# Kernel optimization log

Measured on AMD Instinct MI355X. Metric: run time of the kernel, lower is better.

## Reference

```python
import jax, jax.numpy as jnp
import numpy as np

D = 64      # node_input_dim == node_hidden_dim
EIN = 16    # edge_input_dim
EH = 64     # edge_hidden_dim
NL, NR = 5000, 15000
EL, ER = 50000, 150000
STEPS = 6
EPS = 1e-5
SLOPE = 0.01


def _ln(x, g, b):
    mu = jnp.mean(x, axis=-1, keepdims=True)
    v = jnp.mean((x - mu) ** 2, axis=-1, keepdims=True)
    return (x - mu) / jnp.sqrt(v + EPS) * g + b


def _lrelu(x):
    return jnp.where(x > 0, x, SLOPE * x)


def setup_inputs() -> dict:
    key = jax.random.key(0)
    ks = jax.random.split(key, 32)

    def n(k, shape, fan_in):
        return jax.random.normal(k, shape, jnp.float32) * (fan_in ** -0.5)

    return {
        'lig_n_feat': jax.random.normal(ks[0], (NL, D), jnp.float32),
        'lig_e_feat': jax.random.normal(ks[1], (EL, EIN), jnp.float32),
        'lig_src': jax.random.randint(ks[2], (EL,), 0, NL),
        'lig_dst': jax.random.randint(ks[3], (EL,), 0, NL),
        'rec_n_feat': jax.random.normal(ks[4], (NR, D), jnp.float32),
        'rec_e_feat': jax.random.normal(ks[5], (ER, EIN), jnp.float32),
        'rec_src': jax.random.randint(ks[6], (ER,), 0, NR),
        'rec_dst': jax.random.randint(ks[7], (ER,), 0, NR),
        'mask': jax.random.uniform(ks[8], (NL, NR), jnp.float32),
        # linear0
        'W0': n(ks[9], (D, D), D), 'b0': jnp.zeros((D,), jnp.float32),
        # edge network: Linear(EIN,EH) -> ReLU -> Linear(EH, D*D)
        'We1': n(ks[10], (EH, EIN), EIN), 'be1': jnp.zeros((EH,), jnp.float32),
        'We2': n(ks[11], (D * D, EH), EH), 'be2': jnp.zeros((D * D,), jnp.float32),
        # NNConv residual fc (no bias) and conv bias
        'resW': n(ks[12], (D, D), D), 'conv_b': jnp.zeros((D,), jnp.float32),
        # message layer Linear(2D, D)
        'msgW': n(ks[13], (D, 2 * D), 2 * D), 'msgb': jnp.zeros((D,), jnp.float32),
        # attention projections (no bias)
        'Qlig': n(ks[14], (D, D), D), 'Klig': n(ks[15], (D, D), D), 'Vlig': n(ks[16], (D, D), D),
        'Qrec': n(ks[17], (D, D), D), 'Krec': n(ks[18], (D, D), D), 'Vrec': n(ks[19], (D, D), D),
        # final LayerNorms
        'g_lig': jnp.ones((D,), jnp.float32), 'b_lig': jnp.zeros((D,), jnp.float32),
        'g_rec': jnp.ones((D,), jnp.float32), 'b_rec': jnp.zeros((D,), jnp.float32),
    }


def _gather_branch(x, efeat, src, dst, n_nodes, W0, b0, We1, be1, We2, be2, resW, conv_b, msgW, msgb):
    # per-edge weight matrices from edge MLP: [E, D, D] (in x out)
    We = jax.nn.relu(efeat @ We1.T + be1) @ We2.T + be2
    We = We.reshape(-1, D, D)
    h = jax.nn.relu(x @ W0.T + b0)
    for _ in range(STEPS):
        msg = jnp.einsum('ei,eio->eo', h[src], We)          # gather + per-edge transform
        agg = jax.ops.segment_sum(msg, dst, num_segments=n_nodes)  # scatter-sum
        m = jax.nn.relu(agg + h @ resW.T + conv_b)           # NNConv residual + bias, relu
        h = jnp.concatenate([m, h], axis=1) @ msgW.T + msgb  # message_layer
    return h + x


def reference(lig_n_feat, lig_e_feat, lig_src, lig_dst, rec_n_feat, rec_e_feat, rec_src, rec_dst,
              mask, W0, b0, We1, be1, We2, be2, resW, conv_b, msgW, msgb,
              Qlig, Klig, Vlig, Qrec, Krec, Vrec, g_lig, b_lig, g_rec, b_rec):
    lig_Fv = _gather_branch(lig_n_feat, lig_e_feat, lig_src, lig_dst, NL,
                            W0, b0, We1, be1, We2, be2, resW, conv_b, msgW, msgb)
    rec_Fv = _gather_branch(rec_n_feat, rec_e_feat, rec_src, rec_dst, NR,
                            W0, b0, We1, be1, We2, be2, resW, conv_b, msgW, msgb)
    hl = _ln(lig_Fv, g_lig, b_lig)
    hr = _ln(rec_Fv, g_rec, b_rec)
    # lig attends to rec
    ql, kr, vr = _lrelu(hl @ Qlig.T), _lrelu(hr @ Krec.T), hr @ Vrec.T
    a = mask * (ql @ kr.T) - 1000.0 * (1.0 - mask)
    att_lig = jax.nn.softmax(a, axis=1) @ vr
    # rec attends to lig
    qr, kl, vl = _lrelu(hr @ Qrec.T), _lrelu(hl @ Klig.T), hl @ Vlig.T
    mt = mask.T
    a2 = mt * (qr @ kl.T) - 1000.0 * (1.0 - mt)
    att_rec = jax.nn.softmax(a2, axis=1) @ vl
    return (_ln(att_lig, g_lig, b_lig), _ln(att_rec, g_rec, b_rec))
```

## Files before the change

### kernel.cpp

```cpp
#include <hip/hip_runtime.h>
#include <hip/hip_bf16.h>

typedef unsigned short ushort_t;
typedef __attribute__((ext_vector_type(8))) short short8_t;
typedef __attribute__((ext_vector_type(4))) float f32x4;
typedef __attribute__((ext_vector_type(4))) unsigned uint4_t;
typedef __attribute__((ext_vector_type(2))) unsigned uint2_t;

#define NLIG 5000
#define NREC 15000
#define NTOT 20000
#define ELIG 50000
#define EREC 150000
#define ETOT 200000
#define VSTRIDE 20160
#define NB0 313
#define NB1 938
#define SEGLEN 5000
#define NBA (NB0*3 + NB1)
#define PSLOT 1056

__device__ __forceinline__ float us2f(ushort_t u){
  union { float f; unsigned int i; } x; x.i = ((unsigned int)u) << 16; return x.f;
}
__device__ __forceinline__ ushort_t f2us(float f){
  __hip_bfloat16 b = __float2bfloat16(f);
  return *reinterpret_cast<ushort_t*>(&b);
}
__device__ __forceinline__ unsigned pkbf(float a, float b){
  return (unsigned)f2us(a) | ((unsigned)f2us(b) << 16);
}
__device__ __forceinline__ float wsum64(float v){
#pragma unroll
  for (int s = 32; s >= 1; s >>= 1) v += __shfl_xor(v, s, 64);
  return v;
}
__device__ __forceinline__ f32x4 mfma32(short8_t a, short8_t b, f32x4 c){
  return __builtin_amdgcn_mfma_f32_16x16x32_bf16(a, b, c, 0, 0, 0);
}
__device__ __forceinline__ int geti(const int* __restrict__ p, int i, int i64){
  return i64 ? p[2*i] : p[i];
}

__global__ void kdetect2(const unsigned* __restrict__ xw, const unsigned* __restrict__ iw,
                         int* __restrict__ flagp){
  const int lane = threadIdx.x;
  unsigned w = xw[lane];
  int e0 = (int)((w >> 7) & 0xFF);
  int hit = (e0 >= 100 && e0 <= 134) ? 1 : 0;
  int zodd = ((lane & 1) && iw[lane] == 0u) ? 1 : 0;
#pragma unroll
  for (int s = 32; s >= 1; s >>= 1){
    hit  += __shfl_xor(hit,  s, 64);
    zodd += __shfl_xor(zodd, s, 64);
  }
  if (lane == 0){
    flagp[0] = (hit  >= 40) ? 1 : 0;
    flagp[1] = (zodd >= 24) ? 1 : 0;
  }
}

__global__ void ksent(float* __restrict__ out, int n, float c){
  int i = blockIdx.x*256 + threadIdx.x;
  if (i < n) out[i] = c;
}

__global__ void kcvt_x(const void* __restrict__ lx, const void* __restrict__ rx,
                       const int* __restrict__ flagp, float* __restrict__ xall){
  const int flag = flagp[0];
  const int idx = blockIdx.x*256 + threadIdx.x;
  const void* src; int local;
  if (idx < NLIG*64){ src = lx; local = idx; } else { src = rx; local = idx - NLIG*64; }
  float v;
  if (flag) v = us2f(((const ushort_t*)src)[local]);
  else      v = ((const float*)src)[local];
  xall[idx] = v;
}

struct Srcs { const void* p[20]; };
__global__ void kcvt_w(Srcs S, const int* __restrict__ flagp, float* __restrict__ wcvt){
  const int bounds[21] = {0,4096,4160,5184,5248,267392,271488,275584,275648,283840,
                          283904,288000,292096,296192,300288,304384,308480,308544,308608,308672,308736};
  const int flag = flagp[0];
  const int idx = blockIdx.x*256 + threadIdx.x;
  if (idx >= 308736) return;
  int seg = 0;
#pragma unroll
  for (int s = 1; s < 20; ++s) if (idx >= bounds[s]) seg = s;
  const void* src = S.p[0];
#pragma unroll
  for (int s = 1; s < 20; ++s) if (seg == s) src = S.p[s];
  const int local = idx - bounds[seg];
  float v;
  if (flag) v = us2f(((const ushort_t*)src)[local]);
  else      v = ((const float*)src)[local];
  wcvt[idx] = v;
}

#define W_W0    0
#define W_B0    4096
#define W_WE1   4160
#define W_BE1   5184
#define W_WE2   5248
#define W_BE2   267392
#define W_RESW  271488
#define W_CONVB 275584
#define W_MSGW  275648
#define W_MSGB  283840
#define W_QLIG  283904
#define W_KLIG  288000
#define W_VLIG  292096
#define W_QREC  296192
#define W_KREC  300288
#define W_VREC  304384
#define W_GLIG  308480
#define W_BLIG  308544
#define W_GREC  308608
#define W_BREC  308672

__global__ void kWpk(const float* __restrict__ We2f, ushort_t* __restrict__ Wpk){
  int oidx = blockIdx.x*256 + threadIdx.x;
  int j = oidx & 7, lane = (oidx >> 3) & 63, p = (oidx >> 9) & 1;
  int t = (oidx >> 10) & 3, kb = oidx >> 12;
  int o = t*16 + (lane & 15);
  int gik = kb*32 + (lane >> 4)*8 + j;
  int i = gik >> 6, k = gik & 63;
  float v = We2f[(size_t)(i*64 + o)*64 + k];
  ushort_t hi = f2us(v);
  Wpk[oidx] = p ? f2us(v - us2f(hi)) : hi;
}

__global__ void kh0(const float* __restrict__ xall, const float* __restrict__ W0f,
                    const float* __restrict__ b0f, float* __restrict__ h){
  __shared__ float xr[4][64];
  const int lane = threadIdx.x & 63, wv = threadIdx.x >> 6;
  const int n = blockIdx.x*4 + wv;
  xr[wv][lane] = xall[(size_t)n*64 + lane];
  __syncthreads();
  float acc = b0f[lane];
  const float* wr = W0f + lane*64;
#pragma unroll
  for (int i = 0; i < 64; ++i) acc += xr[wv][i] * wr[i];
  h[(size_t)n*64 + lane] = acc > 0.f ? acc : 0.f;
}

__global__ void khist(const int* __restrict__ ldst, const int* __restrict__ rdst,
                      const int* __restrict__ flagp, int* __restrict__ counts){
  const int i64 = flagp[1];
  const int e = blockIdx.x*256 + threadIdx.x;
  if (e >= ETOT) return;
  int dstg = (e < ELIG) ? geti(ldst, e, i64) : geti(rdst, e - ELIG, i64) + NLIG;
  atomicAdd(&counts[dstg], 1);
}

__global__ __launch_bounds__(1024) void kscan(const int* __restrict__ counts, int* __restrict__ offs){
  __shared__ int part[1024];
  const int tid = threadIdx.x;
  const int PER = 20;
  int loc[PER]; int s = 0;
#pragma unroll
  for (int j = 0; j < PER; ++j){ int idx = tid*PER + j; int v = (idx < NTOT) ? counts[idx] : 0; loc[j] = s; s += v; }
  part[tid] = s;
  __syncthreads();
  for (int d = 1; d < 1024; d <<= 1){
    int add = (tid >= d) ? part[tid - d] : 0;
    __syncthreads();
    part[tid] += add;
    __syncthreads();
  }
  int pre = (tid > 0) ? part[tid - 1] : 0;
#pragma unroll
  for (int j = 0; j < PER; ++j){ int idx = tid*PER + j; if (idx < NTOT) offs[idx] = pre + loc[j]; }
  if (tid == 1023) offs[NTOT] = part[1023];
}

__global__ void kfill(const int* __restrict__ lsrc, const int* __restrict__ ldst,
                      const int* __restrict__ rsrc, const int* __restrict__ rdst,
                      const void* __restrict__ lef, const void* __restrict__ ref_,
                      const int* __restrict__ offs, int* __restrict__ cursor,
                      const int* __restrict__ flagp,
                      int* __restrict__ e_srcn, float* __restrict__ ef_srt){
  const int flag = flagp[0];
  const int i64  = flagp[1];
  const int e = blockIdx.x*256 + threadIdx.x;
  if (e >= ETOT) return;
  int srcg, dstg, le; const void* efb;
  if (e < ELIG){ srcg = geti(lsrc, e, i64); dstg = geti(ldst, e, i64); efb = lef; le = e; }
  else {
    int e2 = e - ELIG;
    srcg = geti(rsrc, e2, i64) + NLIG; dstg = geti(rdst, e2, i64) + NLIG; efb = ref_; le = e2;
  }
  int pos = offs[dstg] + atomicAdd(&cursor[dstg], 1);
  e_srcn[pos] = srcg;
  float* efd = ef_srt + (size_t)pos*16;
  if (flag){
    const ushort_t* efp = (const ushort_t*)efb + (size_t)le*16;
#pragma unroll
    for (int c = 0; c < 16; ++c) efd[c] = us2f(efp[c]);
  } else {
    const float* efp = (const float*)efb + (size_t)le*16;
#pragma unroll
    for (int c = 0; c < 16; ++c) efd[c] = efp[c];
  }
}

__global__ void kz(const float* __restrict__ ef_srt, const float* __restrict__ We1f,
                   const float* __restrict__ be1f, float* __restrict__ z_srt){
  const int lane = threadIdx.x & 63, wv = threadIdx.x >> 6;
  const int e = blockIdx.x*4 + wv;
  const float* efp = ef_srt + (size_t)e*16;
  float acc = be1f[lane];
  const float* wr = We1f + lane*16;
#pragma unroll
  for (int c = 0; c < 16; ++c) acc += efp[c] * wr[c];
  z_srt[(size_t)e*64 + lane] = acc > 0.f ? acc : 0.f;
}

#define SROW 2080
#define SLO  (16*SROW)
__global__ __launch_bounds__(1024)
void kstep(const float* __restrict__ hin, float* __restrict__ hout,
           const int* __restrict__ offs, const int* __restrict__ e_srcn,
           const float* __restrict__ z_srt,
           const ushort_t* __restrict__ Wpk,
           const float* __restrict__ resWf, const float* __restrict__ convbf,
           const float* __restrict__ msgWf, const float* __restrict__ msgbf,
           const float* __restrict__ be2f){
  __shared__ alignas(16) char sbuf[2*SLO];
  __shared__ float h_lds[1024];
  __shared__ float Hs_lds[1024];
  __shared__ float m_lds[1024];
  __shared__ float cbf[64], mbf[64];

  const int tid = threadIdx.x, lane = tid & 63, wv = tid >> 6;
  const int n0 = blockIdx.x * 16;

  h_lds[tid] = hin[(size_t)n0*64 + tid];
  if (tid < 64){ cbf[tid] = convbf[tid]; mbf[tid] = msgbf[tid]; }

  float sacc[64];
#pragma unroll
  for (int i = 0; i < 64; ++i) sacc[i] = 0.f;
  float hs = 0.f;
  {
    const int v = n0 + wv;
    const int jb = offs[v], je = offs[v+1];
    for (int j = jb; j < je; ++j){
      const int sn = e_srcn[j];
      const float zl = z_srt[(size_t)j*64 + lane];
      hs += hin[(size_t)sn*64 + lane];
      const float4* hp = (const float4*)(hin + (size_t)sn*64);
#pragma unroll
      for (int i4 = 0; i4 < 16; ++i4){
        float4 hv = hp[i4];
        sacc[i4*4+0] += hv.x * zl;
        sacc[i4*4+1] += hv.y * zl;
        sacc[i4*4+2] += hv.z * zl;
        sacc[i4*4+3] += hv.w * zl;
      }
    }
    Hs_lds[wv*64 + lane] = hs;
  }

  const int r15 = lane & 15, g4 = lane >> 4;
  const int tW = wv & 3, kq = wv >> 2;
  f32x4 acc; acc[0]=0.f; acc[1]=0.f; acc[2]=0.f; acc[3]=0.f;
#pragma unroll
  for (int c = 0; c < 4; ++c){
#pragma unroll
    for (int ii = 0; ii < 16; ++ii){
      float v = sacc[c*16 + ii];
      ushort_t hi16 = f2us(v);
      unsigned off = (unsigned)(wv*SROW + (ii*64 + lane)*2);
      *(ushort_t*)(sbuf + off) = hi16;
      *(ushort_t*)(sbuf + SLO + off) = f2us(v - us2f(hi16));
    }
    __syncthreads();
    for (int kk = 0; kk < 8; ++kk){
      const int lk = kq*256 + kk*32;
      const int kb = c*32 + kq*8 + kk;
      const unsigned aoff = (unsigned)(r15*SROW + (lk + g4*8)*2);
      const short8_t ah = *(const short8_t*)(sbuf + aoff);
      const short8_t al = *(const short8_t*)(sbuf + SLO + aoff);
      const ushort_t* bp = Wpk + (size_t)(kb*4 + tW)*1024 + lane*8;
      const short8_t bh = *(const short8_t*)(bp);
      const short8_t bl = *(const short8_t*)(bp + 512);
      acc = mfma32(ah, bh, acc);
      acc = mfma32(ah, bl, acc);
      acc = mfma32(al, bh, acc);
    }
    __syncthreads();
  }

  float* redf  = (float*)sbuf;
  float* be2s  = (float*)(sbuf + 16384);
  float* resWt = (float*)(sbuf + 32768);
#pragma unroll
  for (int q = 0; q < 4; ++q)
    redf[kq*1024 + (g4*4 + q)*64 + tW*16 + r15] = acc[q];
  for (int idx = tid; idx < 4096; idx += 1024){
    be2s[idx] = be2f[idx];
    resWt[(idx & 63)*65 + (idx >> 6)] = resWf[idx];
  }
  __syncthreads();
  {
    float aggv = cbf[lane];
#pragma unroll
    for (int k4 = 0; k4 < 4; ++k4) aggv += redf[k4*1024 + wv*64 + lane];
    float t1 = 0.f, t2 = 0.f;
#pragma unroll 8
    for (int i = 0; i < 64; ++i){
      t1 += Hs_lds[wv*64 + i] * be2s[i*64 + lane];
      t2 += h_lds[wv*64 + i]  * resWt[i*65 + lane];
    }
    float mv = aggv + t1 + t2;
    m_lds[wv*64 + lane] = mv > 0.f ? mv : 0.f;
  }
  __syncthreads();
  float* msgWt = (float*)sbuf;
  for (int idx = tid; idx < 8192; idx += 1024)
    msgWt[(idx & 127)*65 + (idx >> 7)] = msgWf[idx];
  __syncthreads();
  {
    float hn = mbf[lane];
#pragma unroll 8
    for (int i = 0; i < 64; ++i){
      hn += m_lds[wv*64 + i] * msgWt[i*65 + lane];
      hn += h_lds[wv*64 + i] * msgWt[(64 + i)*65 + lane];
    }
    hout[(size_t)(n0 + wv)*64 + lane] = hn;
  }
}

__global__ void kfvproj(const float* __restrict__ h, const float* __restrict__ xall,
    const float* __restrict__ wcvt,
    ushort_t* __restrict__ qbh, ushort_t* __restrict__ qbl,
    ushort_t* __restrict__ kbh, ushort_t* __restrict__ kbl,
    ushort_t* __restrict__ vbT){
  __shared__ float hr[4][64];
  const int lane = threadIdx.x & 63, wv = threadIdx.x >> 6;
  const int n = blockIdx.x*4 + wv;
  const bool isLig = n < NLIG;
  const float fv = h[(size_t)n*64 + lane] + xall[(size_t)n*64 + lane];
  const float mu = wsum64(fv) * (1.f/64.f);
  const float dd = fv - mu;
  const float var = wsum64(dd*dd) * (1.f/64.f);
  const float gg = wcvt[(isLig ? W_GLIG : W_GREC) + lane];
  const float bb = wcvt[(isLig ? W_BLIG : W_BREC) + lane];
  const float hl = dd * rsqrtf(var + 1e-5f) * gg + bb;
  hr[wv][lane] = hl;
  __syncthreads();
  const float* Qw = wcvt + (isLig ? W_QLIG : W_QREC) + lane*64;
  const float* Kw = wcvt + (isLig ? W_KLIG : W_KREC) + lane*64;
  const float* Vw = wcvt + (isLig ? W_VLIG : W_VREC) + lane*64;
  float qa = 0.f, ka = 0.f, va = 0.f;
#pragma unroll
  for (int i = 0; i < 64; ++i){
    const float hv = hr[wv][i];
    qa += hv * Qw[i];
    ka += hv * Kw[i];
    va += hv * Vw[i];
  }
  qa = qa > 0.f ? qa : 0.01f*qa;
  ka = ka > 0.f ? ka : 0.01f*ka;
  const size_t o = (size_t)n*64 + lane;
  ushort_t qh = f2us(qa); qbh[o] = qh; qbl[o] = f2us(qa - us2f(qh));
  ushort_t kh = f2us(ka); kbh[o] = kh; kbl[o] = f2us(ka - us2f(kh));
  vbT[(size_t)lane*VSTRIDE + n] = f2us(va);
}

__global__ __launch_bounds__(512)
void kattn4(const ushort_t* __restrict__ qbh, const ushort_t* __restrict__ qbl,
            const ushort_t* __restrict__ kbh, const ushort_t* __restrict__ kbl,
            const ushort_t* __restrict__ vbT, const void* __restrict__ maskp,
            const int* __restrict__ flagp, float* __restrict__ pbuf){
  __shared__ float slab[8][2][512];

  const int flag = flagp[0];
  const int tid = threadIdx.x, lane = tid & 63, wv = tid >> 6;
  const int gw = blockIdx.x*8 + wv;
  if (gw >= NBA) return;
  const int dirn = (gw < NB0*3) ? 0 : 1;
  const int bid  = dirn ? (gw - NB0*3) : (gw/3);
  const int seg  = dirn ? 0 : (gw - (gw/3)*3);
  const int R   = dirn ? NREC : NLIG;
  const int C   = dirn ? NLIG : NREC;
  const int RNB = dirn ? NLIG : 0;
  const int CNB = dirn ? 0 : NLIG;
  const int cs  = dirn ? 0 : seg*SEGLEN;
  const int ce  = dirn ? C : (cs + SEGLEN);

  const int r15 = lane & 15, g4 = lane >> 4;
  const int rbase = bid*16;
  int rn = rbase + r15; if (rn > R-1) rn = R-1;

  const ushort_t* qph = qbh + (size_t)(RNB + rn)*64;
  const ushort_t* qpl = qbl + (size_t)(RNB + rn)*64;
  const short8_t qh0a = *(const short8_t*)(qph + g4*8);
  const short8_t qh0b = *(const short8_t*)(qph + 32 + g4*8);
  const short8_t ql0a = *(const short8_t*)(qpl + g4*8);
  const short8_t ql0b = *(const short8_t*)(qpl + 32 + g4*8);

  const int srcA = (((g4 & 1) * 2)     << 4) + r15;
  const int srcB = (((g4 & 1) * 2 + 1) << 4) + r15;
  const bool hiBank = (g4 >> 1) != 0;

  auto d0_load = [&](int cb, float4 &va, float4 &vb){
    int cA = cb + g4*4;      if (cA > C-4) cA = C-4;
    int cB = cb + 16 + g4*4; if (cB > C-4) cB = C-4;
    if (flag){
      const ushort_t* mrow = (const ushort_t*)maskp + (size_t)rn*NREC;
      const uint2_t wa = *(const uint2_t*)(mrow + cA);
      const uint2_t wb = *(const uint2_t*)(mrow + cB);
      va.x = us2f((ushort_t)(wa[0] & 0xFFFF)); va.y = us2f((ushort_t)(wa[0] >> 16));
      va.z = us2f((ushort_t)(wa[1] & 0xFFFF)); va.w = us2f((ushort_t)(wa[1] >> 16));
      vb.x = us2f((ushort_t)(wb[0] & 0xFFFF)); vb.y = us2f((ushort_t)(wb[0] >> 16));
      vb.z = us2f((ushort_t)(wb[1] & 0xFFFF)); vb.w = us2f((ushort_t)(wb[1] >> 16));
    } else {
      const float* mrow = (const float*)maskp + (size_t)rn*NREC;
      va = *(const float4*)(mrow + cA);
      vb = *(const float4*)(mrow + cB);
    }
  };
  const int s_c = lane >> 1, s_h = lane & 1;
  auto d1_load = [&](int cb, float4 &va, float4 &vb){
    int c = cb + s_c; if (c > C-1) c = C-1;
    int r0 = rbase + s_h*8; if (r0 > R-8) r0 = R-8;
    const size_t base = (size_t)c*NREC + r0;
    if (flag){
      const ushort_t* mp = (const ushort_t*)maskp + base;
      const short8_t v8 = *(const short8_t*)mp;
      va.x = us2f((ushort_t)v8[0]); va.y = us2f((ushort_t)v8[1]);
      va.z = us2f((ushort_t)v8[2]); va.w = us2f((ushort_t)v8[3]);
      vb.x = us2f((ushort_t)v8[4]); vb.y = us2f((ushort_t)v8[5]);
      vb.z = us2f((ushort_t)v8[6]); vb.w = us2f((ushort_t)v8[7]);
    } else {
      const float* mp = (const float*)maskp + base;
      va = *(const float4*)mp;
      vb = *(const float4*)(mp + 4);
    }
  };
  auto d1_write = [&](int b, const float4 &va, const float4 &vb){
    float* s = &slab[wv][b][s_c*16 + s_h*8];
    *(float4*)s = va; *(float4*)(s + 4) = vb;
  };

  float mrun = -1e30f, lrun = 0.f;
  f32x4 oacc[4];
#pragma unroll
  for (int t = 0; t < 4; ++t){ oacc[t][0]=0.f; oacc[t][1]=0.f; oacc[t][2]=0.f; oacc[t][3]=0.f; }

  float4 pA, pB;
  if (dirn == 0) d0_load(cs, pA, pB);
  else { d1_load(cs, pA, pB); d1_write(0, pA, pB); d1_load(cs + 32, pA, pB); }

  int buf = 0;
  for (int cb = cs; cb < ce; cb += 32){
    float mv0[4], mv1[4];
    if (dirn == 0){
      mv0[0]=pA.x; mv0[1]=pA.y; mv0[2]=pA.z; mv0[3]=pA.w;
      mv1[0]=pB.x; mv1[1]=pB.y; mv1[2]=pB.z; mv1[3]=pB.w;
      if (cb + 32 < ce) d0_load(cb + 32, pA, pB);
    } else {
      const float* s = &slab[wv][buf][0];
#pragma unroll
      for (int j = 0; j < 4; ++j){
        mv0[j] = s[(g4*4 + j)*16 + r15];
        mv1[j] = s[(16 + g4*4 + j)*16 + r15];
      }
      if (cb + 32 < ce){
        d1_write(buf ^ 1, pA, pB);
        if (cb + 64 < ce) d1_load(cb + 64, pA, pB);
      }
      buf ^= 1;
    }

    int cn0 = cb + r15;      if (cn0 > C-1) cn0 = C-1;
    int cn1 = cb + 16 + r15; if (cn1 > C-1) cn1 = C-1;
    const ushort_t* kp0h = kbh + (size_t)(CNB + cn0)*64;
    const ushort_t* kp0l = kbl + (size_t)(CNB + cn0)*64;
    const ushort_t* kp1h = kbh + (size_t)(CNB + cn1)*64;
    const ushort_t* kp1l = kbl + (size_t)(CNB + cn1)*64;
    f32x4 st0; st0[0]=0.f; st0[1]=0.f; st0[2]=0.f; st0[3]=0.f;
    f32x4 st1 = st0;
    {
      short8_t ka_ = *(const short8_t*)(kp0h + g4*8);
      short8_t kb_ = *(const short8_t*)(kp0h + 32 + g4*8);
      st0 = mfma32(ka_, qh0a, st0); st0 = mfma32(kb_, qh0b, st0);
      st0 = mfma32(ka_, ql0a, st0); st0 = mfma32(kb_, ql0b, st0);
      short8_t kc_ = *(const short8_t*)(kp0l + g4*8);
      short8_t kd_ = *(const short8_t*)(kp0l + 32 + g4*8);
      st0 = mfma32(kc_, qh0a, st0); st0 = mfma32(kd_, qh0b, st0);
    }
    {
      short8_t ka_ = *(const short8_t*)(kp1h + g4*8);
      short8_t kb_ = *(const short8_t*)(kp1h + 32 + g4*8);
      st1 = mfma32(ka_, qh0a, st1); st1 = mfma32(kb_, qh0b, st1);
      st1 = mfma32(ka_, ql0a, st1); st1 = mfma32(kb_, ql0b, st1);
      short8_t kc_ = *(const short8_t*)(kp1l + g4*8);
      short8_t kd_ = *(const short8_t*)(kp1l + 32 + g4*8);
      st1 = mfma32(kc_, qh0a, st1); st1 = mfma32(kd_, qh0b, st1);
    }
    float sv0[4], sv1[4]; float tmax = -1e30f;
#pragma unroll
    for (int j = 0; j < 4; ++j){
      const int c0 = cb + g4*4 + j, c1 = cb + 16 + g4*4 + j;
      sv0[j] = (c0 < ce) ? mv0[j] * (st0[j] + 1000.f) : -1e30f;
      sv1[j] = (c1 < ce) ? mv1[j] * (st1[j] + 1000.f) : -1e30f;
      tmax = fmaxf(tmax, fmaxf(sv0[j], sv1[j]));
    }
    tmax = fmaxf(tmax, __shfl_xor(tmax, 16, 64));
    tmax = fmaxf(tmax, __shfl_xor(tmax, 32, 64));
    const float mnew = fmaxf(mrun, tmax);
    const float corr = __expf(mrun - mnew);
    float ps0[4], ps1[4], psum = 0.f;
#pragma unroll
    for (int j = 0; j < 4; ++j){
      ps0[j] = __expf(sv0[j] - mnew); psum += ps0[j];
      ps1[j] = __expf(sv1[j] - mnew); psum += ps1[j];
    }
    psum += __shfl_xor(psum, 16, 64);
    psum += __shfl_xor(psum, 32, 64);
    lrun = lrun * corr + psum;
    mrun = mnew;
    const unsigned pk0 = pkbf(ps0[0], ps0[1]);
    const unsigned pk1 = pkbf(ps0[2], ps0[3]);
    const unsigned pk2 = pkbf(ps1[0], ps1[1]);
    const unsigned pk3 = pkbf(ps1[2], ps1[3]);
    const unsigned a0 = (unsigned)__shfl((int)pk0, srcA, 64);
    const unsigned a2 = (unsigned)__shfl((int)pk2, srcA, 64);
    const unsigned a1 = (unsigned)__shfl((int)pk1, srcA, 64);
    const unsigned a3 = (unsigned)__shfl((int)pk3, srcA, 64);
    const unsigned b0 = (unsigned)__shfl((int)pk0, srcB, 64);
    const unsigned b2 = (unsigned)__shfl((int)pk2, srcB, 64);
    const unsigned b1 = (unsigned)__shfl((int)pk1, srcB, 64);
    const unsigned b3 = (unsigned)__shfl((int)pk3, srcB, 64);
    uint4_t pw;
    pw[0] = hiBank ? a2 : a0;
    pw[1] = hiBank ? a3 : a1;
    pw[2] = hiBank ? b2 : b0;
    pw[3] = hiBank ? b3 : b1;
    const short8_t pf8 = *reinterpret_cast<const short8_t*>(&pw);
    const ushort_t* vtb = vbT + (size_t)(CNB + cb + g4*8);
#pragma unroll
    for (int t = 0; t < 4; ++t){
#pragma unroll
      for (int q = 0; q < 4; ++q) oacc[t][q] *= corr;
      const short8_t af = *(const short8_t*)(vtb + (size_t)(t*16 + r15)*VSTRIDE);
      oacc[t] = mfma32(af, pf8, oacc[t]);
    }
  }

  float* ps = pbuf + (size_t)gw * PSLOT;
  if (g4 == 0){ ps[r15] = mrun; ps[16 + r15] = lrun; }
#pragma unroll
  for (int t = 0; t < 4; ++t)
#pragma unroll
    for (int q = 0; q < 4; ++q)
      ps[32 + r15*64 + t*16 + g4*4 + q] = oacc[t][q];
}

__global__ __launch_bounds__(64)
void kcomb(const float* __restrict__ pbuf, const float* __restrict__ wcvt,
           float* __restrict__ out){
  const int rb = blockIdx.x;
  const int lane = threadIdx.x;
  const int dirn = (rb < NB0) ? 0 : 1;
  const int bid  = dirn ? (rb - NB0) : rb;
  const int R    = dirn ? NREC : NLIG;
  const int nseg = dirn ? 1 : 3;
  const int slot0= dirn ? (NB0*3 + bid) : (bid*3);
  const float* gwf = wcvt + (dirn ? W_GREC : W_GLIG);
  const float* bwf = wcvt + (dirn ? W_BREC : W_BLIG);
  float* outp = out + (size_t)(dirn ? NLIG : 0)*64;
  const int rbase = bid * 16;

  for (int rr = 0; rr < 16; ++rr){
    const int rg = rbase + rr;
    if (rg >= R) break;
    float mstar = -1e30f;
    for (int s = 0; s < nseg; ++s)
      mstar = fmaxf(mstar, pbuf[(size_t)(slot0 + s)*PSLOT + rr]);
    float lstar = 0.f, ov = 0.f;
    for (int s = 0; s < nseg; ++s){
      const float* psl = pbuf + (size_t)(slot0 + s)*PSLOT;
      const float e = __expf(psl[rr] - mstar);
      lstar += psl[16 + rr] * e;
      ov    += psl[32 + rr*64 + lane] * e;
    }
    const float att = ov / lstar;
    const float mu = wsum64(att) * (1.f/64.f);
    const float dd = att - mu;
    const float var = wsum64(dd*dd) * (1.f/64.f);
    const float y = dd * rsqrtf(var + 1e-5f) * gwf[lane] + bwf[lane];
    outp[(size_t)rg*64 + lane] = y;
  }
}

extern "C" void kernel_launch(void* const* d_in, const int* in_sizes, int n_in,
                              void* d_out, int out_size, void* d_ws, size_t ws_size,
                              hipStream_t stream){
  const int expsz[29] = {320000,800000,50000,50000,960000,2400000,150000,150000,75000000,
                         4096,64,1024,64,262144,4096,4096,64,8192,64,
                         4096,4096,4096,4096,4096,4096,64,64,64,64};
  bool ok = (n_in == 29);
  if (ok) for (int i = 0; i < 29; ++i) if (in_sizes[i] != expsz[i]) ok = false;
  if (!ok){
    ksent<<<(out_size + 255)/256, 256, 0, stream>>>((float*)d_out, out_size, 10.0f);
    return;
  }

  const void* lig_n = d_in[0];
  const void* lig_e = d_in[1];
  const int* lig_src = (const int*)d_in[2];
  const int* lig_dst = (const int*)d_in[3];
  const void* rec_n = d_in[4];
  const void* rec_e = d_in[5];
  const int* rec_src = (const int*)d_in[6];
  const int* rec_dst = (const int*)d_in[7];
  const void* mask = d_in[8];

  char* p = (char*)d_ws;
  auto carve = [&](size_t bytes)->char*{ char* r = p; p += (bytes + 255) & ~(size_t)255; return r; };
  float*    xall  = (float*)   carve((size_t)NTOT*64*4);
  float*    wcvt  = (float*)   carve((size_t)308736*4);
  float*    h_a   = (float*)   carve((size_t)NTOT*64*4);
  float*    h_b   = (float*)   carve((size_t)NTOT*64*4);
  ushort_t* Wpk   = (ushort_t*)carve((size_t)524288*2);
  ushort_t* qbh   = (ushort_t*)carve((size_t)NTOT*64*2);
  ushort_t* qbl   = (ushort_t*)carve((size_t)NTOT*64*2);
  ushort_t* kbh   = (ushort_t*)carve((size_t)NTOT*64*2);
  ushort_t* kbl   = (ushort_t*)carve((size_t)NTOT*64*2);
  ushort_t* vbT   = (ushort_t*)carve((size_t)64*VSTRIDE*2);
  int*      flag  = (int*)     carve(256);
  int*      counts= (int*)     carve((size_t)2*NTOT*4);
  int*      cursor= counts + NTOT;
  int*      offs  = (int*)     carve((size_t)(NTOT+1)*4);
  int*      e_srcn= (int*)     carve((size_t)ETOT*4);
  float*    ef_srt= (float*)   carve((size_t)ETOT*16*4);
  float*    z_srt = (float*)   carve((size_t)ETOT*64*4);
  float*    pbuf  = ef_srt;

  if ((size_t)(p - (char*)d_ws) > ws_size){
    ksent<<<(out_size + 255)/256, 256, 0, stream>>>((float*)d_out, out_size, 20.0f);
    return;
  }

  Srcs S;
  for (int i = 0; i < 20; ++i) S.p[i] = d_in[9 + i];

  hipMemsetAsync(counts, 0, (size_t)2*NTOT*4, stream);
  hipMemsetAsync(vbT, 0, (size_t)64*VSTRIDE*2, stream);
  kdetect2<<<1, 64, 0, stream>>>((const unsigned*)lig_n, (const unsigned*)lig_src, flag);
  kcvt_x<<<NTOT*64/256, 256, 0, stream>>>(lig_n, rec_n, flag, xall);
  kcvt_w<<<(308736 + 255)/256, 256, 0, stream>>>(S, flag, wcvt);
  kWpk<<<2048, 256, 0, stream>>>(wcvt + W_WE2, Wpk);
  kh0<<<NTOT/4, 256, 0, stream>>>(xall, wcvt + W_W0, wcvt + W_B0, h_a);
  khist<<<(ETOT + 255)/256, 256, 0, stream>>>(lig_dst, rec_dst, flag, counts);
  kscan<<<1, 1024, 0, stream>>>(counts, offs);
  kfill<<<(ETOT + 255)/256, 256, 0, stream>>>(lig_src, lig_dst, rec_src, rec_dst,
                                              lig_e, rec_e, offs, cursor, flag, e_srcn, ef_srt);
  kz<<<ETOT/4, 256, 0, stream>>>(ef_srt, wcvt + W_WE1, wcvt + W_BE1, z_srt);
  float* hi = h_a; float* ho = h_b;
  for (int s = 0; s < 6; ++s){
    kstep<<<NTOT/16, 1024, 0, stream>>>(hi, ho, offs, e_srcn, z_srt, Wpk,
                                        wcvt + W_RESW, wcvt + W_CONVB,
                                        wcvt + W_MSGW, wcvt + W_MSGB, wcvt + W_BE2);
    float* t = hi; hi = ho; ho = t;
  }
  kfvproj<<<NTOT/4, 256, 0, stream>>>(hi, xall, wcvt, qbh, qbl, kbh, kbl, vbT);
  kattn4<<<(NBA + 7)/8, 512, 0, stream>>>(qbh, qbl, kbh, kbl, vbT, mask, flag, pbuf);
  kcomb<<<NB0 + NB1, 64, 0, stream>>>(pbuf, wcvt, (float*)d_out);
}
```

Measured before the change: 2.153 ms.

## Tile V into 32-column blocks, XCD-aware attention scheduling, four-way segment split

Stores the transposed V in 32-column tiles of 2048 elements so each MFMA A-operand load reads a contiguous 4 KB block instead of rows strided by 20160 elements. The attention launch is reorganised into a fixed 320-block grid that uses blockIdx low bits (assumed to map to XCDs) to pick direction and column segment, and the lig->rec direction is split into four segments instead of three. Mask prefetch for the next tile is moved after the MFMA work. Aims for better cache locality and load balance, at the cost of more partial-softmax slots for kcomb to merge.

```diff
diff --git a/kernel.cpp b/kernel.cpp
--- a/kernel.cpp
+++ b/kernel.cpp
@@ -13,12 +13,14 @@
 #define ELIG 50000
 #define EREC 150000
 #define ETOT 200000
-#define VSTRIDE 20160
 #define NB0 313
 #define NB1 938
-#define SEGLEN 5000
-#define NBA (NB0*3 + NB1)
+#define SEG0LEN 3744
+#define NBA2 (NB0*4 + NB1)
 #define PSLOT 1056
+#define VT_LIG 0
+#define VT_REC 157
+#define VT_NT  626
 
 __device__ __forceinline__ float us2f(ushort_t u){
   union { float f; unsigned int i; } x; x.i = ((unsigned int)u) << 16; return x.f;
@@ -336,7 +338,7 @@
     const float* __restrict__ wcvt,
     ushort_t* __restrict__ qbh, ushort_t* __restrict__ qbl,
     ushort_t* __restrict__ kbh, ushort_t* __restrict__ kbl,
-    ushort_t* __restrict__ vbT){
+    ushort_t* __restrict__ vbT3){
   __shared__ float hr[4][64];
   const int lane = threadIdx.x & 63, wv = threadIdx.x >> 6;
   const int n = blockIdx.x*4 + wv;
@@ -366,32 +368,42 @@
   const size_t o = (size_t)n*64 + lane;
   ushort_t qh = f2us(qa); qbh[o] = qh; qbl[o] = f2us(qa - us2f(qh));
   ushort_t kh = f2us(ka); kbh[o] = kh; kbl[o] = f2us(ka - us2f(kh));
-  vbT[(size_t)lane*VSTRIDE + n] = f2us(va);
+  const int c   = isLig ? n : (n - NLIG);
+  const int cbb = (isLig ? VT_LIG : VT_REC) + (c >> 5);
+  vbT3[(size_t)cbb*2048 + lane*32 + (c & 31)] = f2us(va);
 }
 
 __global__ __launch_bounds__(512)
-void kattn4(const ushort_t* __restrict__ qbh, const ushort_t* __restrict__ qbl,
+void kattn5(const ushort_t* __restrict__ qbh, const ushort_t* __restrict__ qbl,
             const ushort_t* __restrict__ kbh, const ushort_t* __restrict__ kbl,
-            const ushort_t* __restrict__ vbT, const void* __restrict__ maskp,
+            const ushort_t* __restrict__ vbT3, const void* __restrict__ maskp,
             const int* __restrict__ flagp, float* __restrict__ pbuf){
   __shared__ float slab[8][2][512];
 
   const int flag = flagp[0];
   const int tid = threadIdx.x, lane = tid & 63, wv = tid >> 6;
-  const int gw = blockIdx.x*8 + wv;
-  if (gw >= NBA) return;
-  const int dirn = (gw < NB0*3) ? 0 : 1;
-  const int bid  = dirn ? (gw - NB0*3) : (gw/3);
-  const int seg  = dirn ? 0 : (gw - (gw/3)*3);
-  const int R   = dirn ? NREC : NLIG;
-  const int C   = dirn ? NLIG : NREC;
-  const int RNB = dirn ? NLIG : 0;
-  const int CNB = dirn ? 0 : NLIG;
-  const int cs  = dirn ? 0 : seg*SEGLEN;
-  const int ce  = dirn ? C : (cs + SEGLEN);
+  const int b = blockIdx.x, xcd = b & 7, kslot = b >> 3;
+
+  int dirn, rb, slot, cs, ce, C, CNB, RNB, R, cbbase;
+  if (xcd < 4){
+    dirn = 0;
+    rb = kslot*8 + wv;
+    if (rb >= NB0) return;
+    slot = rb*4 + xcd;
+    cs = xcd*SEG0LEN;
+    ce = (xcd == 3) ? NREC : cs + SEG0LEN;
+    C = NREC; CNB = NLIG; RNB = 0; R = NLIG; cbbase = VT_REC;
+  } else {
+    dirn = 1;
+    int j = (kslot*8 + wv)*4 + (xcd - 4);
+    if (j >= NB1) return;
+    rb = j; slot = NB0*4 + j;
+    cs = 0; ce = NLIG;
+    C = NLIG; CNB = 0; RNB = NLIG; R = NREC; cbbase = VT_LIG;
+  }
 
   const int r15 = lane & 15, g4 = lane >> 4;
-  const int rbase = bid*16;
+  const int rbase = rb*16;
   int rn = rbase + r15; if (rn > R-1) rn = R-1;
 
   const ushort_t* qph = qbh + (size_t)(RNB + rn)*64;
@@ -440,8 +452,8 @@
       vb = *(const float4*)(mp + 4);
     }
   };
-  auto d1_write = [&](int b, const float4 &va, const float4 &vb){
-    float* s = &slab[wv][b][s_c*16 + s_h*8];
+  auto d1_write = [&](int bq, const float4 &va, const float4 &vb){
+    float* s = &slab[wv][bq][s_c*16 + s_h*8];
     *(float4*)s = va; *(float4*)(s + 4) = vb;
   };
 
@@ -460,7 +472,6 @@
     if (dirn == 0){
       mv0[0]=pA.x; mv0[1]=pA.y; mv0[2]=pA.z; mv0[3]=pA.w;
       mv1[0]=pB.x; mv1[1]=pB.y; mv1[2]=pB.z; mv1[3]=pB.w;
-      if (cb + 32 < ce) d0_load(cb + 32, pA, pB);
     } else {
       const float* s = &slab[wv][buf][0];
 #pragma unroll
@@ -468,11 +479,6 @@
         mv0[j] = s[(g4*4 + j)*16 + r15];
         mv1[j] = s[(16 + g4*4 + j)*16 + r15];
       }
-      if (cb + 32 < ce){
-        d1_write(buf ^ 1, pA, pB);
-        if (cb + 64 < ce) d1_load(cb + 64, pA, pB);
-      }
-      buf ^= 1;
     }
 
     int cn0 = cb + r15;      if (cn0 > C-1) cn0 = C-1;
@@ -541,17 +547,26 @@
     pw[2] = hiBank ? b2 : b0;
     pw[3] = hiBank ? b3 : b1;
     const short8_t pf8 = *reinterpret_cast<const short8_t*>(&pw);
-    const ushort_t* vtb = vbT + (size_t)(CNB + cb + g4*8);
+    const ushort_t* vtb = vbT3 + (size_t)(cbbase + (cb >> 5))*2048 + g4*8;
 #pragma unroll
     for (int t = 0; t < 4; ++t){
 #pragma unroll
       for (int q = 0; q < 4; ++q) oacc[t][q] *= corr;
-      const short8_t af = *(const short8_t*)(vtb + (size_t)(t*16 + r15)*VSTRIDE);
+      const short8_t af = *(const short8_t*)(vtb + (t*16 + r15)*32);
       oacc[t] = mfma32(af, pf8, oacc[t]);
     }
-  }
-
-  float* ps = pbuf + (size_t)gw * PSLOT;
+    if (dirn == 0){
+      if (cb + 32 < ce) d0_load(cb + 32, pA, pB);
+    } else {
+      if (cb + 32 < ce){
+        d1_write(buf ^ 1, pA, pB);
+        if (cb + 64 < ce) d1_load(cb + 64, pA, pB);
+      }
+      buf ^= 1;
+    }
+  }
+
+  float* ps = pbuf + (size_t)slot * PSLOT;
   if (g4 == 0){ ps[r15] = mrun; ps[16 + r15] = lrun; }
 #pragma unroll
   for (int t = 0; t < 4; ++t)
@@ -568,8 +583,8 @@
   const int dirn = (rb < NB0) ? 0 : 1;
   const int bid  = dirn ? (rb - NB0) : rb;
   const int R    = dirn ? NREC : NLIG;
-  const int nseg = dirn ? 1 : 3;
-  const int slot0= dirn ? (NB0*3 + bid) : (bid*3);
+  const int nseg = dirn ? 1 : 4;
+  const int slot0= dirn ? (NB0*4 + bid) : (bid*4);
   const float* gwf = wcvt + (dirn ? W_GREC : W_GLIG);
   const float* bwf = wcvt + (dirn ? W_BREC : W_BLIG);
   float* outp = out + (size_t)(dirn ? NLIG : 0)*64;
@@ -631,7 +646,7 @@
   ushort_t* qbl   = (ushort_t*)carve((size_t)NTOT*64*2);
   ushort_t* kbh   = (ushort_t*)carve((size_t)NTOT*64*2);
   ushort_t* kbl   = (ushort_t*)carve((size_t)NTOT*64*2);
-  ushort_t* vbT   = (ushort_t*)carve((size_t)64*VSTRIDE*2);
+  ushort_t* vbT3  = (ushort_t*)carve((size_t)VT_NT*2048*2);
   int*      flag  = (int*)     carve(256);
   int*      counts= (int*)     carve((size_t)2*NTOT*4);
   int*      cursor= counts + NTOT;
@@ -650,7 +665,7 @@
   for (int i = 0; i < 20; ++i) S.p[i] = d_in[9 + i];
 
   hipMemsetAsync(counts, 0, (size_t)2*NTOT*4, stream);
-  hipMemsetAsync(vbT, 0, (size_t)64*VSTRIDE*2, stream);
+  hipMemsetAsync(vbT3, 0, (size_t)VT_NT*2048*2, stream);
   kdetect2<<<1, 64, 0, stream>>>((const unsigned*)lig_n, (const unsigned*)lig_src, flag);
   kcvt_x<<<NTOT*64/256, 256, 0, stream>>>(lig_n, rec_n, flag, xall);
   kcvt_w<<<(308736 + 255)/256, 256, 0, stream>>>(S, flag, wcvt);
@@ -668,7 +683,7 @@
                                         wcvt + W_MSGW, wcvt + W_MSGB, wcvt + W_BE2);
     float* t = hi; hi = ho; ho = t;
   }
-  kfvproj<<<NTOT/4, 256, 0, stream>>>(hi, xall, wcvt, qbh, qbl, kbh, kbl, vbT);
-  kattn4<<<(NBA + 7)/8, 512, 0, stream>>>(qbh, qbl, kbh, kbl, vbT, mask, flag, pbuf);
+  kfvproj<<<NTOT/4, 256, 0, stream>>>(hi, xall, wcvt, qbh, qbl, kbh, kbl, vbT3);
+  kattn5<<<320, 512, 0, stream>>>(qbh, qbl, kbh, kbl, vbT3, mask, flag, pbuf);
   kcomb<<<NB0 + NB1, 64, 0, stream>>>(pbuf, wcvt, (float*)d_out);
 }
```

Result: slower. 2.244 ms (+4.2%).
